# Performance work log

Hardware: AMD Instinct MI355X
Metric: run time of the kernel (lower is better)

Reference implementation:

```python
import jax, jax.numpy as jnp
import numpy as np

D = 2048
N_DRUG, N_PROT = 10000, 20000
E = 100000


def setup_inputs() -> dict:
    key = jax.random.key(0)
    ks = jax.random.split(key, 10)
    return {
        "x_drug": jax.random.normal(ks[0], (N_DRUG, D), dtype=jnp.float32),
        "x_protein": jax.random.normal(ks[1], (N_PROT, D), dtype=jnp.float32),
        "rel_ddi": jax.random.normal(ks[2], (D,), dtype=jnp.float32),
        "rel_dpi": jax.random.normal(ks[3], (D,), dtype=jnp.float32),
        "ddi_src": jax.random.randint(ks[4], (E,), 0, N_DRUG, dtype=jnp.int64 if jax.config.jax_enable_x64 else jnp.int32),
        "ddi_dst": jax.random.randint(ks[5], (E,), 0, N_DRUG, dtype=jnp.int64 if jax.config.jax_enable_x64 else jnp.int32),
        "dpi_src": jax.random.randint(ks[6], (E,), 0, N_DRUG, dtype=jnp.int64 if jax.config.jax_enable_x64 else jnp.int32),
        "dpi_dst": jax.random.randint(ks[7], (E,), 0, N_PROT, dtype=jnp.int64 if jax.config.jax_enable_x64 else jnp.int32),
        "ppi_src": jax.random.randint(ks[8], (E,), 0, N_PROT, dtype=jnp.int64 if jax.config.jax_enable_x64 else jnp.int32),
        "ppi_dst": jax.random.randint(ks[9], (E,), 0, N_PROT, dtype=jnp.int64 if jax.config.jax_enable_x64 else jnp.int32),
    }


def _edge_score(x_src, x_dst, src, dst, rel):
    # gather [E, D] head/tail, DistMult-style multiply-reduce, clamp to [0, 1]
    head = x_src[src]
    tail = x_dst[dst]
    score = jnp.sum(head * rel * tail, axis=-1)
    return jnp.clip(score, 0.0, 1.0)


def reference(x_drug, x_protein, rel_ddi, rel_dpi,
              ddi_src, ddi_dst, dpi_src, dpi_dst, ppi_src, ppi_dst):
    score_ddi = _edge_score(x_drug, x_drug, ddi_src, ddi_dst, rel_ddi)
    score_dpi = _edge_score(x_drug, x_protein, dpi_src, dpi_dst, rel_dpi)
    # NOTE: original module (faithfully) applies the DPI relation to PPI edges
    score_ppi = _edge_score(x_protein, x_protein, ppi_src, ppi_dst, rel_dpi)
    return (score_ddi, score_dpi, score_ppi)
```

## Files before the change

kernel.cpp:

```cpp
#include <hip/hip_runtime.h>

#define D4 512
#define K_EDGES 16


__global__ void zero_ints(int* __restrict__ p, int n) {
    int i = blockIdx.x * blockDim.x + threadIdx.x;
    if (i < n) p[i] = 0;
}

__global__ void hist3(const int* __restrict__ s0, const int* __restrict__ s1,
                      const int* __restrict__ s2, int E,
                      int* __restrict__ cnt, int nd) {
    int i = blockIdx.x * blockDim.x + threadIdx.x;
    const int total = 3 * E;
    for (; i < total; i += gridDim.x * blockDim.x) {
        if (i < E)           atomicAdd(&cnt[s0[i]], 1);
        else if (i < 2 * E)  atomicAdd(&cnt[nd + s1[i - E]], 1);
        else                 atomicAdd(&cnt[2 * nd + s2[i - 2 * E]], 1);
    }
}

__global__ void scan3(const int* __restrict__ cnt, int* __restrict__ base,
                      int nd, int np) {
    __shared__ int part[1024];
    const int b = blockIdx.x;
    const int off = (b == 0) ? 0 : (b == 1) ? nd : 2 * nd;
    const int N = (b == 2) ? np : nd;
    const int t = threadIdx.x;
    const int C = (N + blockDim.x - 1) / blockDim.x;
    const int lo = t * C, hi = min(lo + C, N);
    int s = 0;
    for (int i = lo; i < hi; ++i) s += cnt[off + i];
    part[t] = s;
    __syncthreads();
    if (t == 0) {
        int run = 0;
        for (int i = 0; i < (int)blockDim.x; ++i) { int tmp = part[i]; part[i] = run; run += tmp; }
    }
    __syncthreads();
    int run = part[t];
    for (int i = lo; i < hi; ++i) { base[off + i] = run; run += cnt[off + i]; }
}

__global__ void scatter3(const int* __restrict__ s0, const int* __restrict__ s1,
                         const int* __restrict__ s2, int E,
                         int* __restrict__ base, int nd, int* __restrict__ sorted) {
    int i = blockIdx.x * blockDim.x + threadIdx.x;
    const int total = 3 * E;
    for (; i < total; i += gridDim.x * blockDim.x) {
        if (i < E)          { int p = atomicAdd(&base[s0[i]], 1);           sorted[p] = i; }
        else if (i < 2 * E) { int k = i - E;     int p = atomicAdd(&base[nd + s1[k]], 1);     sorted[E + p] = k; }
        else                { int k = i - 2 * E; int p = atomicAdd(&base[2 * nd + s2[k]], 1); sorted[2 * E + p] = k; }
    }
}

__global__ __launch_bounds__(256) void score_sorted(
    const float4* __restrict__ xdrug, const float4* __restrict__ xprot,
    const float4* __restrict__ rddi,  const float4* __restrict__ rdpi,
    const int* __restrict__ ddi_src, const int* __restrict__ ddi_dst,
    const int* __restrict__ dpi_src, const int* __restrict__ dpi_dst,
    const int* __restrict__ ppi_src, const int* __restrict__ ppi_dst,
    const int* __restrict__ sorted, float* __restrict__ out, int E)
{
    const int lane = threadIdx.x & 63;
    const int wpb = blockDim.x >> 6;
    int wid = blockIdx.x * wpb + (threadIdx.x >> 6);
    const int nw = gridDim.x * wpb;
    const int cpr = (E + K_EDGES - 1) / K_EDGES;
    const int total_chunks = 3 * cpr;

    for (int c = wid; c < total_chunks; c += nw) {
        const int r = c / cpr;
        const int ci = c - r * cpr;
        const int e_lo = ci * K_EDGES;
        const int e_hi = min(e_lo + K_EDGES, E);

        const float4 *xs, *xd, *rel;
        const int *srcA, *dstA, *sl;
        float* o;
        if (r == 0)      { xs = xdrug; xd = xdrug; rel = rddi; srcA = ddi_src; dstA = ddi_dst; sl = sorted;         o = out; }
        else if (r == 1) { xs = xdrug; xd = xprot; rel = rdpi; srcA = dpi_src; dstA = dpi_dst; sl = sorted + E;     o = out + E; }
        else             { xs = xprot; xd = xprot; rel = rdpi; srcA = ppi_src; dstA = ppi_dst; sl = sorted + 2 * E; o = out + 2 * E; }

        float4 rr[8];
#pragma unroll
        for (int j = 0; j < 8; ++j) rr[j] = rel[j * 64 + lane];

        int cur_src = -1;
        float4 hr[8];
        for (int i = e_lo; i < e_hi; ++i) {
            const int e = sl[i];
            const int s = srcA[e];
            if (s != cur_src) {
                cur_src = s;
                const float4* __restrict__ hp = xs + (size_t)s * D4;
#pragma unroll
                for (int j = 0; j < 8; ++j) {
                    float4 h = hp[j * 64 + lane];
                    hr[j].x = h.x * rr[j].x;
                    hr[j].y = h.y * rr[j].y;
                    hr[j].z = h.z * rr[j].z;
                    hr[j].w = h.w * rr[j].w;
                }
            }
            const int d = dstA[e];
            const float4* __restrict__ tp = xd + (size_t)d * D4;
            float acc = 0.f;
#pragma unroll
            for (int j = 0; j < 8; ++j) {
                float4 t = tp[j * 64 + lane];
                acc = fmaf(hr[j].x, t.x, acc);
                acc = fmaf(hr[j].y, t.y, acc);
                acc = fmaf(hr[j].z, t.z, acc);
                acc = fmaf(hr[j].w, t.w, acc);
            }
#pragma unroll
            for (int off = 32; off; off >>= 1) acc += __shfl_down(acc, off, 64);
            if (lane == 0) o[e] = fminf(fmaxf(acc, 0.f), 1.f);
        }
    }
}

__global__ __launch_bounds__(256) void edge_score_all(
    const float4* __restrict__ xdrug, const float4* __restrict__ xprot,
    const float4* __restrict__ rddi,  const float4* __restrict__ rdpi,
    const int* __restrict__ ddi_src, const int* __restrict__ ddi_dst,
    const int* __restrict__ dpi_src, const int* __restrict__ dpi_dst,
    const int* __restrict__ ppi_src, const int* __restrict__ ppi_dst,
    float* __restrict__ out, int E)
{
    __shared__ float4 srel[2][D4];
    for (int i = threadIdx.x; i < D4; i += blockDim.x) {
        srel[0][i] = rddi[i];
        srel[1][i] = rdpi[i];
    }
    __syncthreads();
    const int lane = threadIdx.x & 63;
    const int wpb = blockDim.x >> 6;
    int wid = blockIdx.x * wpb + (threadIdx.x >> 6);
    const int nw = gridDim.x * wpb;
    const int total = 3 * E;
    for (int e = wid; e < total; e += nw) {
        const float4 *hp, *tp;
        int sel;
        if (e < E)          { hp = xdrug + (size_t)ddi_src[e] * D4; tp = xdrug + (size_t)ddi_dst[e] * D4; sel = 0; }
        else if (e < 2 * E) { int k = e - E;     hp = xdrug + (size_t)dpi_src[k] * D4; tp = xprot + (size_t)dpi_dst[k] * D4; sel = 1; }
        else                { int k = e - 2 * E; hp = xprot + (size_t)ppi_src[k] * D4; tp = xprot + (size_t)ppi_dst[k] * D4; sel = 1; }
        float acc = 0.f;
#pragma unroll
        for (int j = 0; j < 8; ++j) {
            const int idx = j * 64 + lane;
            float4 h = hp[idx], t = tp[idx], r = srel[sel][idx];
            acc = fmaf(h.x * r.x, t.x, acc);
            acc = fmaf(h.y * r.y, t.y, acc);
            acc = fmaf(h.z * r.z, t.z, acc);
            acc = fmaf(h.w * r.w, t.w, acc);
        }
#pragma unroll
        for (int off = 32; off; off >>= 1) acc += __shfl_down(acc, off, 64);
        if (lane == 0) out[e] = fminf(fmaxf(acc, 0.f), 1.f);
    }
}

extern "C" void kernel_launch(void* const* d_in, const int* in_sizes, int n_in,
                              void* d_out, int out_size, void* d_ws, size_t ws_size,
                              hipStream_t stream) {
    const float* x_drug    = (const float*)d_in[0];
    const float* x_protein = (const float*)d_in[1];
    const float* rel_ddi   = (const float*)d_in[2];
    const float* rel_dpi   = (const float*)d_in[3];
    const int* ddi_src = (const int*)d_in[4];
    const int* ddi_dst = (const int*)d_in[5];
    const int* dpi_src = (const int*)d_in[6];
    const int* dpi_dst = (const int*)d_in[7];
    const int* ppi_src = (const int*)d_in[8];
    const int* ppi_dst = (const int*)d_in[9];

    const int D  = in_sizes[2];
    const int nd = in_sizes[0] / D;
    const int np = in_sizes[1] / D;
    const int E  = in_sizes[4];
    float* out = (float*)d_out;

    const int CB = 2 * nd + np;
    const size_t need = (size_t)(2 * CB + 3 * E) * sizeof(int);

    if (ws_size < need) {
        edge_score_all<<<2048, 256, 0, stream>>>(
            (const float4*)x_drug, (const float4*)x_protein,
            (const float4*)rel_ddi, (const float4*)rel_dpi,
            ddi_src, ddi_dst, dpi_src, dpi_dst, ppi_src, ppi_dst, out, E);
        return;
    }

    int* cnt    = (int*)d_ws;
    int* base   = cnt + CB;
    int* sorted = base + CB;

    zero_ints<<<(CB + 255) / 256, 256, 0, stream>>>(cnt, CB);
    hist3<<<1024, 256, 0, stream>>>(ddi_src, dpi_src, ppi_src, E, cnt, nd);
    scan3<<<3, 1024, 0, stream>>>(cnt, base, nd, np);
    scatter3<<<1024, 256, 0, stream>>>(ddi_src, dpi_src, ppi_src, E, base, nd, sorted);

    const int cpr = (E + K_EDGES - 1) / K_EDGES;
    const int total_chunks = 3 * cpr;
    const int waves_per_block = 4;
    const int blocks = (total_chunks + waves_per_block - 1) / waves_per_block;

    score_sorted<<<blocks, 256, 0, stream>>>(
        (const float4*)x_drug, (const float4*)x_protein,
        (const float4*)rel_ddi, (const float4*)rel_dpi,
        ddi_src, ddi_dst, dpi_src, dpi_dst, ppi_src, ppi_dst,
        sorted, out, E);
}
```

Baseline: 711.2 us.

## Double-buffer tail-row gathers and stage relation vectors in shared memory

Restructures the sorted-edge scoring loop to prefetch the next edge's tail row into a second register buffer while the current edge is scored, overlapping gather latency with compute. Relation vectors are now staged in LDS per block instead of held in registers per chunk. The edge chunk size doubles to raise head-row reuse per wave. Holding two tail buffers plus the head row raises register pressure and may cut occupancy, and larger chunks mean fewer waves.

```diff
diff --git a/kernel.cpp b/kernel.cpp
--- a/kernel.cpp
+++ b/kernel.cpp
@@ -1,7 +1,7 @@
 #include <hip/hip_runtime.h>
 
 #define D4 512
-#define K_EDGES 16
+#define K_EDGES 32
 
 
 __global__ void zero_ints(int* __restrict__ p, int n) {
@@ -63,6 +63,13 @@
     const int* __restrict__ ppi_src, const int* __restrict__ ppi_dst,
     const int* __restrict__ sorted, float* __restrict__ out, int E)
 {
+    __shared__ float4 srel[2][D4];
+    for (int i = threadIdx.x; i < D4; i += blockDim.x) {
+        srel[0][i] = rddi[i];
+        srel[1][i] = rdpi[i];
+    }
+    __syncthreads();
+
     const int lane = threadIdx.x & 63;
     const int wpb = blockDim.x >> 6;
     int wid = blockIdx.x * wpb + (threadIdx.x >> 6);
@@ -76,48 +83,78 @@
         const int e_lo = ci * K_EDGES;
         const int e_hi = min(e_lo + K_EDGES, E);
 
-        const float4 *xs, *xd, *rel;
+        const float4 *xs, *xd;
+        const float4* srelp;
         const int *srcA, *dstA, *sl;
         float* o;
-        if (r == 0)      { xs = xdrug; xd = xdrug; rel = rddi; srcA = ddi_src; dstA = ddi_dst; sl = sorted;         o = out; }
-        else if (r == 1) { xs = xdrug; xd = xprot; rel = rdpi; srcA = dpi_src; dstA = dpi_dst; sl = sorted + E;     o = out + E; }
-        else             { xs = xprot; xd = xprot; rel = rdpi; srcA = ppi_src; dstA = ppi_dst; sl = sorted + 2 * E; o = out + 2 * E; }
-
-        float4 rr[8];
-#pragma unroll
-        for (int j = 0; j < 8; ++j) rr[j] = rel[j * 64 + lane];
+        if (r == 0)      { xs = xdrug; xd = xdrug; srelp = srel[0]; srcA = ddi_src; dstA = ddi_dst; sl = sorted;         o = out; }
+        else if (r == 1) { xs = xdrug; xd = xprot; srelp = srel[1]; srcA = dpi_src; dstA = dpi_dst; sl = sorted + E;     o = out + E; }
+        else             { xs = xprot; xd = xprot; srelp = srel[1]; srcA = ppi_src; dstA = ppi_dst; sl = sorted + 2 * E; o = out + 2 * E; }
 
         int cur_src = -1;
         float4 hr[8];
-        for (int i = e_lo; i < e_hi; ++i) {
-            const int e = sl[i];
-            const int s = srcA[e];
-            if (s != cur_src) {
-                cur_src = s;
-                const float4* __restrict__ hp = xs + (size_t)s * D4;
-#pragma unroll
-                for (int j = 0; j < 8; ++j) {
-                    float4 h = hp[j * 64 + lane];
-                    hr[j].x = h.x * rr[j].x;
-                    hr[j].y = h.y * rr[j].y;
-                    hr[j].z = h.z * rr[j].z;
-                    hr[j].w = h.w * rr[j].w;
-                }
-            }
-            const int d = dstA[e];
-            const float4* __restrict__ tp = xd + (size_t)d * D4;
+        float4 tA[8], tB[8];
+
+        auto load_hr = [&](int s) {
+            const float4* __restrict__ hp = xs + (size_t)s * D4;
+#pragma unroll
+            for (int j = 0; j < 8; ++j) {
+                float4 h = hp[j * 64 + lane];
+                float4 rv = srelp[j * 64 + lane];
+                hr[j].x = h.x * rv.x;
+                hr[j].y = h.y * rv.y;
+                hr[j].z = h.z * rv.z;
+                hr[j].w = h.w * rv.w;
+            }
+        };
+        auto score_one = [&](const float4 (&t)[8], int e) {
             float acc = 0.f;
 #pragma unroll
             for (int j = 0; j < 8; ++j) {
-                float4 t = tp[j * 64 + lane];
-                acc = fmaf(hr[j].x, t.x, acc);
-                acc = fmaf(hr[j].y, t.y, acc);
-                acc = fmaf(hr[j].z, t.z, acc);
-                acc = fmaf(hr[j].w, t.w, acc);
+                acc = fmaf(hr[j].x, t[j].x, acc);
+                acc = fmaf(hr[j].y, t[j].y, acc);
+                acc = fmaf(hr[j].z, t[j].z, acc);
+                acc = fmaf(hr[j].w, t[j].w, acc);
             }
 #pragma unroll
             for (int off = 32; off; off >>= 1) acc += __shfl_down(acc, off, 64);
             if (lane == 0) o[e] = fminf(fmaxf(acc, 0.f), 1.f);
+        };
+
+        int i = e_lo;
+        int eA = sl[i];
+        {
+            const float4* __restrict__ tp = xd + (size_t)dstA[eA] * D4;
+#pragma unroll
+            for (int j = 0; j < 8; ++j) tA[j] = tp[j * 64 + lane];
+        }
+
+        while (i < e_hi) {
+            int eB = -1;
+            if (i + 1 < e_hi) {
+                eB = sl[i + 1];
+                const float4* __restrict__ tp = xd + (size_t)dstA[eB] * D4;
+#pragma unroll
+                for (int j = 0; j < 8; ++j) tB[j] = tp[j * 64 + lane];
+            }
+            int s = srcA[eA];
+            if (s != cur_src) { cur_src = s; load_hr(s); }
+            score_one(tA, eA);
+            ++i;
+            if (i >= e_hi) break;
+
+            int eC = -1;
+            if (i + 1 < e_hi) {
+                eC = sl[i + 1];
+                const float4* __restrict__ tp = xd + (size_t)dstA[eC] * D4;
+#pragma unroll
+                for (int j = 0; j < 8; ++j) tA[j] = tp[j * 64 + lane];
+            }
+            s = srcA[eB];
+            if (s != cur_src) { cur_src = s; load_hr(s); }
+            score_one(tB, eB);
+            ++i;
+            eA = eC;
         }
     }
 }
@@ -151,11 +188,11 @@
 #pragma unroll
         for (int j = 0; j < 8; ++j) {
             const int idx = j * 64 + lane;
-            float4 h = hp[idx], t = tp[idx], r = srel[sel][idx];
-            acc = fmaf(h.x * r.x, t.x, acc);
-            acc = fmaf(h.y * r.y, t.y, acc);
-            acc = fmaf(h.z * r.z, t.z, acc);
-            acc = fmaf(h.w * r.w, t.w, acc);
+            float4 h = hp[idx], t = tp[idx], rv = srel[sel][idx];
+            acc = fmaf(h.x * rv.x, t.x, acc);
+            acc = fmaf(h.y * rv.y, t.y, acc);
+            acc = fmaf(h.z * rv.z, t.z, acc);
+            acc = fmaf(h.w * rv.w, t.w, acc);
         }
 #pragma unroll
         for (int off = 32; off; off >>= 1) acc += __shfl_down(acc, off, 64);
```

Result: no change. 711.8 us (+0.1%).

## Bucket DPI edges by protein block before source, enlarge chunks, stage relations in LDS

Applied to the files above, without the earlier changes.

The counting sort for DPI edges now keys on (dst protein block of 4096, src drug), so edges processed together touch a narrower range of protein rows and should get better L2/MALL reuse of tail gathers. Edges per wave chunk double from 16 to 32, so a cached head row is reused across more edges. Relation vectors move into shared memory instead of being held in per-wave registers. The costs are a larger histogram/scan array (nblk*nd entries), scanned serially by a single block, and fewer, longer chunks, which can leave the GPU less evenly loaded.

```diff
diff --git a/kernel.cpp b/kernel.cpp
--- a/kernel.cpp
+++ b/kernel.cpp
@@ -1,7 +1,8 @@
 #include <hip/hip_runtime.h>
 
 #define D4 512
-#define K_EDGES 16
+#define K_EDGES 32
+#define DPI_BLK_SHIFT 12
 
 
 __global__ void zero_ints(int* __restrict__ p, int n) {
@@ -9,24 +10,31 @@
     if (i < n) p[i] = 0;
 }
 
-__global__ void hist3(const int* __restrict__ s0, const int* __restrict__ s1,
+__global__ void hist3(const int* __restrict__ s0,
+                      const int* __restrict__ s1, const int* __restrict__ d1,
                       const int* __restrict__ s2, int E,
-                      int* __restrict__ cnt, int nd) {
+                      int* __restrict__ cnt, int nd, int nblk) {
     int i = blockIdx.x * blockDim.x + threadIdx.x;
     const int total = 3 * E;
     for (; i < total; i += gridDim.x * blockDim.x) {
-        if (i < E)           atomicAdd(&cnt[s0[i]], 1);
-        else if (i < 2 * E)  atomicAdd(&cnt[nd + s1[i - E]], 1);
-        else                 atomicAdd(&cnt[2 * nd + s2[i - 2 * E]], 1);
+        if (i < E) {
+            atomicAdd(&cnt[s0[i]], 1);
+        } else if (i < 2 * E) {
+            int k = i - E;
+            atomicAdd(&cnt[nd + (d1[k] >> DPI_BLK_SHIFT) * nd + s1[k]], 1);
+        } else {
+            int k = i - 2 * E;
+            atomicAdd(&cnt[nd + nblk * nd + s2[k]], 1);
+        }
     }
 }
 
 __global__ void scan3(const int* __restrict__ cnt, int* __restrict__ base,
-                      int nd, int np) {
+                      int nd, int np, int nblk) {
     __shared__ int part[1024];
     const int b = blockIdx.x;
-    const int off = (b == 0) ? 0 : (b == 1) ? nd : 2 * nd;
-    const int N = (b == 2) ? np : nd;
+    const int off = (b == 0) ? 0 : (b == 1) ? nd : nd + nblk * nd;
+    const int N   = (b == 0) ? nd : (b == 1) ? nblk * nd : np;
     const int t = threadIdx.x;
     const int C = (N + blockDim.x - 1) / blockDim.x;
     const int lo = t * C, hi = min(lo + C, N);
@@ -43,15 +51,26 @@
     for (int i = lo; i < hi; ++i) { base[off + i] = run; run += cnt[off + i]; }
 }
 
-__global__ void scatter3(const int* __restrict__ s0, const int* __restrict__ s1,
+__global__ void scatter3(const int* __restrict__ s0,
+                         const int* __restrict__ s1, const int* __restrict__ d1,
                          const int* __restrict__ s2, int E,
-                         int* __restrict__ base, int nd, int* __restrict__ sorted) {
+                         int* __restrict__ base, int nd, int nblk,
+                         int* __restrict__ sorted) {
     int i = blockIdx.x * blockDim.x + threadIdx.x;
     const int total = 3 * E;
     for (; i < total; i += gridDim.x * blockDim.x) {
-        if (i < E)          { int p = atomicAdd(&base[s0[i]], 1);           sorted[p] = i; }
-        else if (i < 2 * E) { int k = i - E;     int p = atomicAdd(&base[nd + s1[k]], 1);     sorted[E + p] = k; }
-        else                { int k = i - 2 * E; int p = atomicAdd(&base[2 * nd + s2[k]], 1); sorted[2 * E + p] = k; }
+        if (i < E) {
+            int p = atomicAdd(&base[s0[i]], 1);
+            sorted[p] = i;
+        } else if (i < 2 * E) {
+            int k = i - E;
+            int p = atomicAdd(&base[nd + (d1[k] >> DPI_BLK_SHIFT) * nd + s1[k]], 1);
+            sorted[E + p] = k;
+        } else {
+            int k = i - 2 * E;
+            int p = atomicAdd(&base[nd + nblk * nd + s2[k]], 1);
+            sorted[2 * E + p] = k;
+        }
     }
 }
 
@@ -63,6 +82,13 @@
     const int* __restrict__ ppi_src, const int* __restrict__ ppi_dst,
     const int* __restrict__ sorted, float* __restrict__ out, int E)
 {
+    __shared__ float4 srel[2][D4];
+    for (int i = threadIdx.x; i < D4; i += blockDim.x) {
+        srel[0][i] = rddi[i];
+        srel[1][i] = rdpi[i];
+    }
+    __syncthreads();
+
     const int lane = threadIdx.x & 63;
     const int wpb = blockDim.x >> 6;
     int wid = blockIdx.x * wpb + (threadIdx.x >> 6);
@@ -76,16 +102,13 @@
         const int e_lo = ci * K_EDGES;
         const int e_hi = min(e_lo + K_EDGES, E);
 
-        const float4 *xs, *xd, *rel;
+        const float4 *xs, *xd;
+        const float4* srelp;
         const int *srcA, *dstA, *sl;
         float* o;
-        if (r == 0)      { xs = xdrug; xd = xdrug; rel = rddi; srcA = ddi_src; dstA = ddi_dst; sl = sorted;         o = out; }
-        else if (r == 1) { xs = xdrug; xd = xprot; rel = rdpi; srcA = dpi_src; dstA = dpi_dst; sl = sorted + E;     o = out + E; }
-        else             { xs = xprot; xd = xprot; rel = rdpi; srcA = ppi_src; dstA = ppi_dst; sl = sorted + 2 * E; o = out + 2 * E; }
-
-        float4 rr[8];
-#pragma unroll
-        for (int j = 0; j < 8; ++j) rr[j] = rel[j * 64 + lane];
+        if (r == 0)      { xs = xdrug; xd = xdrug; srelp = srel[0]; srcA = ddi_src; dstA = ddi_dst; sl = sorted;         o = out; }
+        else if (r == 1) { xs = xdrug; xd = xprot; srelp = srel[1]; srcA = dpi_src; dstA = dpi_dst; sl = sorted + E;     o = out + E; }
+        else             { xs = xprot; xd = xprot; srelp = srel[1]; srcA = ppi_src; dstA = ppi_dst; sl = sorted + 2 * E; o = out + 2 * E; }
 
         int cur_src = -1;
         float4 hr[8];
@@ -97,11 +120,12 @@
                 const float4* __restrict__ hp = xs + (size_t)s * D4;
 #pragma unroll
                 for (int j = 0; j < 8; ++j) {
-                    float4 h = hp[j * 64 + lane];
-                    hr[j].x = h.x * rr[j].x;
-                    hr[j].y = h.y * rr[j].y;
-                    hr[j].z = h.z * rr[j].z;
-                    hr[j].w = h.w * rr[j].w;
+                    float4 h  = hp[j * 64 + lane];
+                    float4 rv = srelp[j * 64 + lane];
+                    hr[j].x = h.x * rv.x;
+                    hr[j].y = h.y * rv.y;
+                    hr[j].z = h.z * rv.z;
+                    hr[j].w = h.w * rv.w;
                 }
             }
             const int d = dstA[e];
@@ -151,11 +175,11 @@
 #pragma unroll
         for (int j = 0; j < 8; ++j) {
             const int idx = j * 64 + lane;
-            float4 h = hp[idx], t = tp[idx], r = srel[sel][idx];
-            acc = fmaf(h.x * r.x, t.x, acc);
-            acc = fmaf(h.y * r.y, t.y, acc);
-            acc = fmaf(h.z * r.z, t.z, acc);
-            acc = fmaf(h.w * r.w, t.w, acc);
+            float4 h = hp[idx], t = tp[idx], rv = srel[sel][idx];
+            acc = fmaf(h.x * rv.x, t.x, acc);
+            acc = fmaf(h.y * rv.y, t.y, acc);
+            acc = fmaf(h.z * rv.z, t.z, acc);
+            acc = fmaf(h.w * rv.w, t.w, acc);
         }
 #pragma unroll
         for (int off = 32; off; off >>= 1) acc += __shfl_down(acc, off, 64);
@@ -183,7 +207,8 @@
     const int E  = in_sizes[4];
     float* out = (float*)d_out;
 
-    const int CB = 2 * nd + np;
+    const int nblk = (np + (1 << DPI_BLK_SHIFT) - 1) >> DPI_BLK_SHIFT;
+    const int CB = nd + nblk * nd + np;
     const size_t need = (size_t)(2 * CB + 3 * E) * sizeof(int);
 
     if (ws_size < need) {
@@ -199,9 +224,9 @@
     int* sorted = base + CB;
 
     zero_ints<<<(CB + 255) / 256, 256, 0, stream>>>(cnt, CB);
-    hist3<<<1024, 256, 0, stream>>>(ddi_src, dpi_src, ppi_src, E, cnt, nd);
-    scan3<<<3, 1024, 0, stream>>>(cnt, base, nd, np);
-    scatter3<<<1024, 256, 0, stream>>>(ddi_src, dpi_src, ppi_src, E, base, nd, sorted);
+    hist3<<<1024, 256, 0, stream>>>(ddi_src, dpi_src, dpi_dst, ppi_src, E, cnt, nd, nblk);
+    scan3<<<3, 1024, 0, stream>>>(cnt, base, nd, np, nblk);
+    scatter3<<<1024, 256, 0, stream>>>(ddi_src, dpi_src, dpi_dst, ppi_src, E, base, nd, nblk, sorted);
 
     const int cpr = (E + K_EDGES - 1) / K_EDGES;
     const int total_chunks = 3 * cpr;
```

New measurement: 779.7 us. 1.1x slower.
